# Optimization experiments

Hardware: AMD Instinct MI355X
Metric: run time of the kernel (lower is better)

The kernel has to match this reference:

```python
import jax, jax.numpy as jnp
import numpy as np

N_NODES = 100000


def gcn_conv(x, edge_index, W, b):
    """PyG GCNConv: add self-loops, symmetric deg^{-1/2} normalization,
    linear transform, scatter-add aggregation, then bias."""
    n = x.shape[0]
    loops = jnp.arange(n, dtype=edge_index.dtype)
    src = jnp.concatenate([edge_index[0], loops])  # [E+N]
    dst = jnp.concatenate([edge_index[1], loops])  # [E+N]
    # degree (with self-loops) of each target node
    deg = jax.ops.segment_sum(jnp.ones_like(dst, dtype=x.dtype), dst, num_segments=n)
    dinv = jnp.where(deg > 0, jax.lax.rsqrt(deg), 0.0)
    norm = dinv[src] * dinv[dst]  # [E+N]
    h = x @ W  # [N, out_dim] -- transform before aggregation
    msg = h[src] * norm[:, None]  # gather + normalize
    out = jax.ops.segment_sum(msg, dst, num_segments=n)  # scatter-add
    return out + b


def setup_inputs() -> dict:
    key = jax.random.key(0)
    ks = jax.random.split(key, 8)
    n, e, d_in, d_h = N_NODES, 1600000, 32, 64
    x = jax.random.normal(ks[0], (n, d_in), dtype=jnp.float32)
    edge_index = jax.random.randint(ks[1], (2, e), 0, n, dtype=jnp.int64)
    # Glorot-style init for GCN weights, uniform for linear layer
    W1 = jax.random.normal(ks[2], (d_in, d_h), dtype=jnp.float32) / np.sqrt(d_in)
    b1 = jnp.zeros((d_h,), dtype=jnp.float32)
    W2 = jax.random.normal(ks[3], (d_h, d_h), dtype=jnp.float32) / np.sqrt(d_h)
    b2 = jnp.zeros((d_h,), dtype=jnp.float32)
    Wo = jax.random.normal(ks[4], (d_h, 1), dtype=jnp.float32) / np.sqrt(d_h)
    bo = jnp.zeros((1,), dtype=jnp.float32)
    return {"x": x, "edge_index": edge_index, "W1": W1, "b1": b1,
            "W2": W2, "b2": b2, "Wo": Wo, "bo": bo}


def reference(x, edge_index, W1, b1, W2, b2, Wo, bo):
    h = jax.nn.relu(gcn_conv(x, edge_index, W1, b1))
    h = jax.nn.relu(gcn_conv(h, edge_index, W2, b2))
    logits = h @ Wo + bo  # [N, 1]
    return jax.nn.sigmoid(logits).squeeze(-1)  # [N]
```

## Files before the change

### kernel.cpp

```cpp
#include <hip/hip_runtime.h>

#define DH 64
#define DIN 32
#define BSH 8
#define BNODES 256
#define MAXB 1024
#define CAPSH 13
#define CAP (1 << CAPSH)

typedef unsigned short u16;
typedef unsigned int u32;
typedef float f32x2 __attribute__((ext_vector_type(2)));

__device__ __forceinline__ float bf2f(u16 u) {
    union { u32 i; float f; } x; x.i = ((u32)u) << 16; return x.f;
}
__device__ __forceinline__ u16 f2bf(float f) {
    union { float f; u32 i; } x; x.f = f;
    u32 r = x.i + 0x7fff + ((x.i >> 16) & 1);
    return (u16)(r >> 16);
}
__device__ __forceinline__ float bfl(u32 u) {
    union { u32 i; float f; } x; x.i = u << 16; return x.f;
}
__device__ __forceinline__ float bfh(u32 u) {
    union { u32 i; float f; } x; x.i = u & 0xffff0000u; return x.f;
}
__device__ __forceinline__ void pkacc(f32x2& a, u32 u) {
    f32x2 b;
    b[0] = bfl(u); b[1] = bfh(u);
    asm("v_pk_add_f32 %0, %1, %0" : "+v"(a) : "v"(b));
}

__global__ void __launch_bounds__(512) binA_k(
        const int* __restrict__ ei, int* __restrict__ gcnt,
        u32* __restrict__ pairs, int E, int n, int nbuck) {
    __shared__ int lhist[MAXB];
    __shared__ int lbase[MAXB];
    __shared__ int smode;
    int t = threadIdx.x;
    if (t < 64) {
        int v = (2 * t + 1 < 2 * E) ? ei[2 * t + 1] : 0;
        unsigned long long b = __ballot(v != 0);
        if (t == 0) smode = (b != 0ULL) ? 1 : 0;
    }
    for (int b = t; b < nbuck; b += 512) lhist[b] = 0;
    __syncthreads();
    int m = smode;
    unsigned un = (unsigned)n;
    int q0 = blockIdx.x * 512 + t;
    int qs = gridDim.x * 512;

    if (m && !(E & 3)) {
        const int4* d4 = (const int4*)(ei + E);
        for (int q = q0; q < (E >> 2); q += qs) {
            int4 d = d4[q];
            if ((unsigned)d.x < un) atomicAdd(&lhist[d.x >> BSH], 1);
            if ((unsigned)d.y < un) atomicAdd(&lhist[d.y >> BSH], 1);
            if ((unsigned)d.z < un) atomicAdd(&lhist[d.z >> BSH], 1);
            if ((unsigned)d.w < un) atomicAdd(&lhist[d.w >> BSH], 1);
        }
    } else if (!m && !(E & 1)) {
        const int4* d4 = (const int4*)(ei + 2 * E);
        for (int q = q0; q < (E >> 1); q += qs) {
            int4 d = d4[q];
            if ((unsigned)d.x < un) atomicAdd(&lhist[d.x >> BSH], 1);
            if ((unsigned)d.z < un) atomicAdd(&lhist[d.z >> BSH], 1);
        }
    } else {
        const int* dstp = m ? (ei + E) : (ei + 2 * E);
        int stride = m ? 1 : 2;
        for (int e = q0; e < E; e += qs) {
            int d = dstp[(size_t)e * stride];
            if ((unsigned)d < un) atomicAdd(&lhist[d >> BSH], 1);
        }
    }
    __syncthreads();
    for (int b = t; b < nbuck; b += 512) {
        int c = lhist[b];
        lbase[b] = c ? ((b << CAPSH) + atomicAdd(&gcnt[b], c)) : 0;
        lhist[b] = 0;
    }
    __syncthreads();
    #define EMIT(S, D)                                                     \
        if ((unsigned)(D) < un) {                                          \
            int sv = ((unsigned)(S) < un) ? (S) : 0;                       \
            int bb = (D) >> BSH;                                           \
            int off = atomicAdd(&lhist[bb], 1);                            \
            int pos = lbase[bb] + off;                                     \
            if (pos < ((bb + 1) << CAPSH))                                 \
                pairs[pos] = ((u32)sv << BSH) | (u32)((D) & (BNODES - 1)); \
        }
    if (m && !(E & 3)) {
        const int4* s4 = (const int4*)ei;
        const int4* d4 = (const int4*)(ei + E);
        for (int q = q0; q < (E >> 2); q += qs) {
            int4 s = s4[q]; int4 d = d4[q];
            EMIT(s.x, d.x) EMIT(s.y, d.y) EMIT(s.z, d.z) EMIT(s.w, d.w)
        }
    } else if (!m && !(E & 1)) {
        const int4* s4 = (const int4*)ei;
        const int4* d4 = (const int4*)(ei + 2 * E);
        for (int q = q0; q < (E >> 1); q += qs) {
            int4 s = s4[q]; int4 d = d4[q];
            EMIT(s.x, d.x) EMIT(s.z, d.z)
        }
    } else {
        const int* srcp = ei;
        const int* dstp = m ? (ei + E) : (ei + 2 * E);
        int stride = m ? 1 : 2;
        for (int e = q0; e < E; e += qs) {
            int d = dstp[(size_t)e * stride];
            int s = srcp[(size_t)e * stride];
            EMIT(s, d)
        }
    }
    #undef EMIT
}

__global__ void __launch_bounds__(512) csr_build_k(
        const u32* __restrict__ pairs, const int* __restrict__ gcnt,
        int* __restrict__ rstart, int* __restrict__ rend,
        int* __restrict__ col, float* __restrict__ dinv, int N) {
    __shared__ int cnt[BNODES];
    __shared__ int s[BNODES];
    int b = blockIdx.x, t = threadIdx.x;
    int base = b << CAPSH;
    int ec = gcnt[b]; if (ec > CAP) ec = CAP;
    int end = base + ec;
    if (t < BNODES) cnt[t] = 0;
    __syncthreads();
    for (int i = base + t; i < end; i += 512)
        atomicAdd(&cnt[pairs[i] & (BNODES - 1)], 1);
    __syncthreads();
    int v = (t < BNODES) ? cnt[t] : 0;
    if (t < BNODES) s[t] = v;
    __syncthreads();
    for (int off = 1; off < BNODES; off <<= 1) {
        int xsc = (t >= off && t < BNODES) ? s[t - off] : 0;
        __syncthreads();
        if (t < BNODES) s[t] += xsc;
        __syncthreads();
    }
    if (t < BNODES) {
        int excl = s[t] - v;
        int a = base + excl;
        int node = (b << BSH) + t;
        if (node < N) {
            rstart[node] = a;
            rend[node]   = a + v;
            dinv[node]   = rsqrtf((float)v + 1.0f);
        }
        cnt[t] = a;
    }
    __syncthreads();
    for (int i = base + t; i < end; i += 512) {
        u32 p = pairs[i];
        int pos = atomicAdd(&cnt[p & (BNODES - 1)], 1);
        col[pos] = (int)((p >> BSH) << 7);
    }
}

__global__ void __launch_bounds__(256) gemm1_k(
        const float* __restrict__ x, const float* __restrict__ W1,
        const float* __restrict__ dinv, u16* __restrict__ hp, int N) {
    __shared__ float Wl[DIN * DH];
    __shared__ float xl[16][DIN + 4];
    int t = threadIdx.x;
    {
        const float4* Wv = (const float4*)W1;
        float4* Wd = (float4*)Wl;
        #pragma unroll
        for (int r = 0; r < 2; r++) Wd[t + 256 * r] = Wv[t + 256 * r];
    }
    if (blockIdx.x == 0 && t < 32)
        ((float*)(hp + (size_t)N * DH))[t] = 0.f;
    if (t < 128) {
        int row = t >> 3, ck = (t & 7) * 4;
        int node = blockIdx.x * 16 + row;
        float4 vx = {0.f, 0.f, 0.f, 0.f};
        if (node < N)
            vx = *(const float4*)&x[(size_t)node * DIN + ck];
        *(float4*)&xl[row][ck] = vx;
    }
    __syncthreads();
    int lane = t & 63, w = t >> 6;
    int g = lane >> 4, c = lane & 15;
    int nl = w * 4 + g;
    int node = blockIdx.x * 16 + nl;
    const float* xr = xl[nl];
    float4 acc = {0.f, 0.f, 0.f, 0.f};
    #pragma unroll
    for (int k = 0; k < DIN; k++) {
        float xv = xr[k];
        float4 wv = *(const float4*)&Wl[k * DH + c * 4];
        acc.x += xv * wv.x; acc.y += xv * wv.y; acc.z += xv * wv.z; acc.w += xv * wv.w;
    }
    if (node < N) {
        float di = dinv[node];
        ushort4 o;
        o.x = f2bf(acc.x * di); o.y = f2bf(acc.y * di);
        o.z = f2bf(acc.z * di); o.w = f2bf(acc.w * di);
        *(ushort4*)&hp[(size_t)node * DH + c * 4] = o;
    }
}

__device__ __forceinline__ void edge_sum8p(const u16* __restrict__ hp,
                                           const int* __restrict__ colb,
                                           int start, int deg, int gl, int c,
                                           int sentb, f32x2* __restrict__ acc) {
    int dm = deg;
    dm = max(dm, __shfl_xor(dm, 8, 64));
    dm = max(dm, __shfl_xor(dm, 16, 64));
    dm = max(dm, __shfl_xor(dm, 32, 64));
    if (dm <= 0) return;
    const char* hpco = (const char*)hp + ((u32)c << 4);
    int cb = (c < deg) ? colb[start + c] : sentb;
    for (int base = 0; base < dm; base += 8) {
        int nb = base + 8;
        int cbn = sentb;
        if (nb < dm) cbn = (nb + c < deg) ? colb[start + nb + c] : sentb;
        int s0 = __shfl(cb, gl | 0, 64);
        int s1 = __shfl(cb, gl | 1, 64);
        int s2 = __shfl(cb, gl | 2, 64);
        int s3 = __shfl(cb, gl | 3, 64);
        int s4 = __shfl(cb, gl | 4, 64);
        int s5 = __shfl(cb, gl | 5, 64);
        int s6 = __shfl(cb, gl | 6, 64);
        int s7 = __shfl(cb, gl | 7, 64);
        uint4 v0 = *(const uint4*)(hpco + s0);
        uint4 v1 = *(const uint4*)(hpco + s1);
        uint4 v2 = *(const uint4*)(hpco + s2);
        uint4 v3 = *(const uint4*)(hpco + s3);
        uint4 v4 = *(const uint4*)(hpco + s4);
        uint4 v5 = *(const uint4*)(hpco + s5);
        uint4 v6 = *(const uint4*)(hpco + s6);
        uint4 v7 = *(const uint4*)(hpco + s7);
        pkacc(acc[0], v0.x); pkacc(acc[1], v0.y); pkacc(acc[2], v0.z); pkacc(acc[3], v0.w);
        pkacc(acc[0], v1.x); pkacc(acc[1], v1.y); pkacc(acc[2], v1.z); pkacc(acc[3], v1.w);
        pkacc(acc[0], v2.x); pkacc(acc[1], v2.y); pkacc(acc[2], v2.z); pkacc(acc[3], v2.w);
        pkacc(acc[0], v3.x); pkacc(acc[1], v3.y); pkacc(acc[2], v3.z); pkacc(acc[3], v3.w);
        pkacc(acc[0], v4.x); pkacc(acc[1], v4.y); pkacc(acc[2], v4.z); pkacc(acc[3], v4.w);
        pkacc(acc[0], v5.x); pkacc(acc[1], v5.y); pkacc(acc[2], v5.z); pkacc(acc[3], v5.w);
        pkacc(acc[0], v6.x); pkacc(acc[1], v6.y); pkacc(acc[2], v6.z); pkacc(acc[3], v6.w);
        pkacc(acc[0], v7.x); pkacc(acc[1], v7.y); pkacc(acc[2], v7.z); pkacc(acc[3], v7.w);
        cb = cbn;
    }
}

__global__ void __launch_bounds__(256) agg1_k(
        const u16* __restrict__ hp, const int* __restrict__ rstart,
        const int* __restrict__ rend, const int* __restrict__ col,
        const float* __restrict__ dinv, const float* __restrict__ b1,
        float* __restrict__ out1, int N) {
    int lane = threadIdx.x & 63;
    int g = lane >> 3, c = lane & 7, gl = g << 3;
    int node = blockIdx.x * 32 + (threadIdx.x >> 6) * 8 + g;
    int start = 0, deg = 0;
    if (node < N) { start = rstart[node]; deg = rend[node] - start; }
    f32x2 acc[4] = {{0.f,0.f},{0.f,0.f},{0.f,0.f},{0.f,0.f}};
    edge_sum8p(hp, col, start, deg, gl, c, N << 7, acc);
    if (node < N) {
        uint4 sv = *(const uint4*)&hp[(size_t)node * DH + c * 8];
        float di = dinv[node];
        float4 blo = *(const float4*)&b1[c * 8];
        float4 bhi = *(const float4*)&b1[c * 8 + 4];
        float4 lo, hi;
        lo.x = fmaxf((acc[0][0] + bfl(sv.x)) * di + blo.x, 0.f);
        lo.y = fmaxf((acc[0][1] + bfh(sv.x)) * di + blo.y, 0.f);
        lo.z = fmaxf((acc[1][0] + bfl(sv.y)) * di + blo.z, 0.f);
        lo.w = fmaxf((acc[1][1] + bfh(sv.y)) * di + blo.w, 0.f);
        hi.x = fmaxf((acc[2][0] + bfl(sv.z)) * di + bhi.x, 0.f);
        hi.y = fmaxf((acc[2][1] + bfh(sv.z)) * di + bhi.y, 0.f);
        hi.z = fmaxf((acc[3][0] + bfl(sv.w)) * di + bhi.z, 0.f);
        hi.w = fmaxf((acc[3][1] + bfh(sv.w)) * di + bhi.w, 0.f);
        *(float4*)&out1[(size_t)node * DH + c * 8]     = lo;
        *(float4*)&out1[(size_t)node * DH + c * 8 + 4] = hi;
    }
}

__global__ void __launch_bounds__(256) gemm2_k(
        const float* __restrict__ out1, const float* __restrict__ W2,
        const float* __restrict__ dinv, u16* __restrict__ hp2, int N) {
    __shared__ float Wl[DH * DH];
    __shared__ float xl[16][DH + 4];
    int t = threadIdx.x;
    {
        const float4* Wv = (const float4*)W2;
        float4* Wd = (float4*)Wl;
        #pragma unroll
        for (int r = 0; r < 4; r++) Wd[t + 256 * r] = Wv[t + 256 * r];
    }
    if (blockIdx.x == 0 && t < 32)
        ((float*)(hp2 + (size_t)N * DH))[t] = 0.f;
    {
        int row = t >> 4, ck = (t & 15) * 4;
        int node = blockIdx.x * 16 + row;
        float4 vx = {0.f, 0.f, 0.f, 0.f};
        if (node < N)
            vx = *(const float4*)&out1[(size_t)node * DH + ck];
        *(float4*)&xl[row][ck] = vx;
    }
    __syncthreads();
    int lane = t & 63, w = t >> 6;
    int g = lane >> 4, c = lane & 15;
    int nl = w * 4 + g;
    int node = blockIdx.x * 16 + nl;
    const float* xr = xl[nl];
    float4 acc = {0.f, 0.f, 0.f, 0.f};
    #pragma unroll
    for (int k = 0; k < DH; k++) {
        float xv = xr[k];
        float4 wv = *(const float4*)&Wl[k * DH + c * 4];
        acc.x += xv * wv.x; acc.y += xv * wv.y; acc.z += xv * wv.z; acc.w += xv * wv.w;
    }
    if (node < N) {
        float di = dinv[node];
        ushort4 o;
        o.x = f2bf(acc.x * di); o.y = f2bf(acc.y * di);
        o.z = f2bf(acc.z * di); o.w = f2bf(acc.w * di);
        *(ushort4*)&hp2[(size_t)node * DH + c * 4] = o;
    }
}

__global__ void __launch_bounds__(256) agg_head_k(
        const u16* __restrict__ hp, const int* __restrict__ rstart,
        const int* __restrict__ rend, const int* __restrict__ col,
        const float* __restrict__ dinv, const float* __restrict__ bias,
        const float* __restrict__ Wo, const float* __restrict__ bo,
        float* __restrict__ y, int N) {
    int lane = threadIdx.x & 63;
    int g = lane >> 3, c = lane & 7, gl = g << 3;
    int node = blockIdx.x * 32 + (threadIdx.x >> 6) * 8 + g;
    int start = 0, deg = 0;
    if (node < N) { start = rstart[node]; deg = rend[node] - start; }
    f32x2 acc[4] = {{0.f,0.f},{0.f,0.f},{0.f,0.f},{0.f,0.f}};
    edge_sum8p(hp, col, start, deg, gl, c, N << 7, acc);
    float t = 0.f;
    if (node < N) {
        uint4 sv = *(const uint4*)&hp[(size_t)node * DH + c * 8];
        float4 blo = *(const float4*)&bias[c * 8];
        float4 bhi = *(const float4*)&bias[c * 8 + 4];
        float4 wlo = *(const float4*)&Wo[c * 8];
        float4 whi = *(const float4*)&Wo[c * 8 + 4];
        float di = dinv[node];
        t = fmaxf((acc[0][0] + bfl(sv.x)) * di + blo.x, 0.f) * wlo.x
          + fmaxf((acc[0][1] + bfh(sv.x)) * di + blo.y, 0.f) * wlo.y
          + fmaxf((acc[1][0] + bfl(sv.y)) * di + blo.z, 0.f) * wlo.z
          + fmaxf((acc[1][1] + bfh(sv.y)) * di + blo.w, 0.f) * wlo.w
          + fmaxf((acc[2][0] + bfl(sv.z)) * di + bhi.x, 0.f) * whi.x
          + fmaxf((acc[2][1] + bfh(sv.z)) * di + bhi.y, 0.f) * whi.y
          + fmaxf((acc[3][0] + bfl(sv.w)) * di + bhi.z, 0.f) * whi.z
          + fmaxf((acc[3][1] + bfh(sv.w)) * di + bhi.w, 0.f) * whi.w;
    }
    t += __shfl_xor(t, 1, 64);
    t += __shfl_xor(t, 2, 64);
    t += __shfl_xor(t, 4, 64);
    if (c == 0 && node < N) {
        float z = t + bo[0];
        y[node] = 1.f / (1.f + __expf(-z));
    }
}

extern "C" void kernel_launch(void* const* d_in, const int* in_sizes, int n_in,
                              void* d_out, int out_size, void* d_ws, size_t ws_size,
                              hipStream_t stream) {
    const float* x  = (const float*)d_in[0];
    const int*   ei = (const int*)d_in[1];
    const float* W1 = (const float*)d_in[2];
    const float* b1 = (const float*)d_in[3];
    const float* W2 = (const float*)d_in[4];
    const float* b2 = (const float*)d_in[5];
    const float* Wo = (const float*)d_in[6];
    const float* bo = (const float*)d_in[7];
    float* y = (float*)d_out;

    int N = in_sizes[0] / DIN;
    int E = in_sizes[1] / 2;
    int nbuck = ((N - 1) >> BSH) + 1;

    char* ws = (char*)d_ws;
    size_t off = 0;
    auto alloc = [&](size_t bytes) { char* p = ws + off; off += (bytes + 255) & ~(size_t)255; return p; };
    int*   gcnt   = (int*)alloc(MAXB * 4);
    int*   rstart = (int*)alloc((size_t)N * 4);
    int*   rend   = (int*)alloc((size_t)N * 4);
    float* dinv   = (float*)alloc((size_t)N * 4);
    int*   col    = (int*)alloc(((size_t)nbuck << CAPSH) * 4);
    size_t pair_b = ((size_t)nbuck << CAPSH) * 4;
    size_t hp_b   = (size_t)N * DH * 2 + 256;
    char*  bufA   = (char*)alloc(pair_b > hp_b ? pair_b : hp_b);
    u16*   bufB   = (u16*)alloc(hp_b);
    float* out1   = (float*)alloc((size_t)N * DH * 4);
    u16*   hp    = (u16*)bufA;
    u32*   pairs = (u32*)bufA;

    hipMemsetAsync(gcnt, 0, (size_t)nbuck * 4, stream);
    binA_k<<<256, 512, 0, stream>>>(ei, gcnt, pairs, E, N, nbuck);
    csr_build_k<<<nbuck, 512, 0, stream>>>(pairs, gcnt, rstart, rend, col, dinv, N);
    gemm1_k<<<(N + 15) / 16, 256, 0, stream>>>(x, W1, dinv, hp, N);
    agg1_k<<<(N + 31) / 32, 256, 0, stream>>>(hp, rstart, rend, col, dinv, b1, out1, N);
    gemm2_k<<<(N + 15) / 16, 256, 0, stream>>>(out1, W2, dinv, bufB, N);
    agg_head_k<<<(N + 31) / 32, 256, 0, stream>>>(bufB, rstart, rend, col, dinv, b2, Wo, bo, y, N);
}
```

Measured before the change: 199.7 us.

## Register-cache CSR pairs, pack row bounds into int2, retune binning grid

The CSR build kernel now runs 1024 threads per bucket. Each thread loads up to eight pair entries into registers once and reuses them for both the counting pass and the scatter pass, so the second global read of pairs goes away. Row start and end are packed into a single int2 array, so each aggregation kernel does one 8-byte load per node. The binning kernel moves from 256 blocks of 512 threads to 1024 blocks of 256, which adds more global atomics on the bucket counters. The register path assumes at most 8192 entries per bucket, which holds because CAP is 8192.

```diff
diff --git a/kernel.cpp b/kernel.cpp
--- a/kernel.cpp
+++ b/kernel.cpp
@@ -32,7 +32,7 @@
     asm("v_pk_add_f32 %0, %1, %0" : "+v"(a) : "v"(b));
 }
 
-__global__ void __launch_bounds__(512) binA_k(
+__global__ void __launch_bounds__(256) binA_k(
         const int* __restrict__ ei, int* __restrict__ gcnt,
         u32* __restrict__ pairs, int E, int n, int nbuck) {
     __shared__ int lhist[MAXB];
@@ -44,12 +44,12 @@
         unsigned long long b = __ballot(v != 0);
         if (t == 0) smode = (b != 0ULL) ? 1 : 0;
     }
-    for (int b = t; b < nbuck; b += 512) lhist[b] = 0;
+    for (int b = t; b < nbuck; b += 256) lhist[b] = 0;
     __syncthreads();
     int m = smode;
     unsigned un = (unsigned)n;
-    int q0 = blockIdx.x * 512 + t;
-    int qs = gridDim.x * 512;
+    int q0 = blockIdx.x * 256 + t;
+    int qs = gridDim.x * 256;
 
     if (m && !(E & 3)) {
         const int4* d4 = (const int4*)(ei + E);
@@ -76,7 +76,7 @@
         }
     }
     __syncthreads();
-    for (int b = t; b < nbuck; b += 512) {
+    for (int b = t; b < nbuck; b += 256) {
         int c = lhist[b];
         lbase[b] = c ? ((b << CAPSH) + atomicAdd(&gcnt[b], c)) : 0;
         lhist[b] = 0;
@@ -118,9 +118,9 @@
     #undef EMIT
 }
 
-__global__ void __launch_bounds__(512) csr_build_k(
+__global__ void __launch_bounds__(1024) csr_build_k(
         const u32* __restrict__ pairs, const int* __restrict__ gcnt,
-        int* __restrict__ rstart, int* __restrict__ rend,
+        int2* __restrict__ rse,
         int* __restrict__ col, float* __restrict__ dinv, int N) {
     __shared__ int cnt[BNODES];
     __shared__ int s[BNODES];
@@ -130,8 +130,24 @@
     int end = base + ec;
     if (t < BNODES) cnt[t] = 0;
     __syncthreads();
-    for (int i = base + t; i < end; i += 512)
-        atomicAdd(&cnt[pairs[i] & (BNODES - 1)], 1);
+    u32 pr0, pr1, pr2, pr3, pr4, pr5, pr6, pr7;
+    #define IDX(K) (base + t + ((K) << 10))
+    pr0 = (IDX(0) < end) ? pairs[IDX(0)] : 0u;
+    pr1 = (IDX(1) < end) ? pairs[IDX(1)] : 0u;
+    pr2 = (IDX(2) < end) ? pairs[IDX(2)] : 0u;
+    pr3 = (IDX(3) < end) ? pairs[IDX(3)] : 0u;
+    pr4 = (IDX(4) < end) ? pairs[IDX(4)] : 0u;
+    pr5 = (IDX(5) < end) ? pairs[IDX(5)] : 0u;
+    pr6 = (IDX(6) < end) ? pairs[IDX(6)] : 0u;
+    pr7 = (IDX(7) < end) ? pairs[IDX(7)] : 0u;
+    if (IDX(0) < end) atomicAdd(&cnt[pr0 & (BNODES - 1)], 1);
+    if (IDX(1) < end) atomicAdd(&cnt[pr1 & (BNODES - 1)], 1);
+    if (IDX(2) < end) atomicAdd(&cnt[pr2 & (BNODES - 1)], 1);
+    if (IDX(3) < end) atomicAdd(&cnt[pr3 & (BNODES - 1)], 1);
+    if (IDX(4) < end) atomicAdd(&cnt[pr4 & (BNODES - 1)], 1);
+    if (IDX(5) < end) atomicAdd(&cnt[pr5 & (BNODES - 1)], 1);
+    if (IDX(6) < end) atomicAdd(&cnt[pr6 & (BNODES - 1)], 1);
+    if (IDX(7) < end) atomicAdd(&cnt[pr7 & (BNODES - 1)], 1);
     __syncthreads();
     int v = (t < BNODES) ? cnt[t] : 0;
     if (t < BNODES) s[t] = v;
@@ -147,18 +163,21 @@
         int a = base + excl;
         int node = (b << BSH) + t;
         if (node < N) {
-            rstart[node] = a;
-            rend[node]   = a + v;
-            dinv[node]   = rsqrtf((float)v + 1.0f);
+            rse[node]  = make_int2(a, a + v);
+            dinv[node] = rsqrtf((float)v + 1.0f);
         }
         cnt[t] = a;
     }
     __syncthreads();
-    for (int i = base + t; i < end; i += 512) {
-        u32 p = pairs[i];
-        int pos = atomicAdd(&cnt[p & (BNODES - 1)], 1);
-        col[pos] = (int)((p >> BSH) << 7);
-    }
+    #define SCAT(PR, K)                                                    \
+        if (IDX(K) < end) {                                                \
+            int pos = atomicAdd(&cnt[(PR) & (BNODES - 1)], 1);             \
+            col[pos] = (int)(((PR) >> BSH) << 7);                          \
+        }
+    SCAT(pr0, 0) SCAT(pr1, 1) SCAT(pr2, 2) SCAT(pr3, 3)
+    SCAT(pr4, 4) SCAT(pr5, 5) SCAT(pr6, 6) SCAT(pr7, 7)
+    #undef SCAT
+    #undef IDX
 }
 
 __global__ void __launch_bounds__(256) gemm1_k(
@@ -249,15 +268,15 @@
 }
 
 __global__ void __launch_bounds__(256) agg1_k(
-        const u16* __restrict__ hp, const int* __restrict__ rstart,
-        const int* __restrict__ rend, const int* __restrict__ col,
+        const u16* __restrict__ hp, const int2* __restrict__ rse,
+        const int* __restrict__ col,
         const float* __restrict__ dinv, const float* __restrict__ b1,
         float* __restrict__ out1, int N) {
     int lane = threadIdx.x & 63;
     int g = lane >> 3, c = lane & 7, gl = g << 3;
     int node = blockIdx.x * 32 + (threadIdx.x >> 6) * 8 + g;
     int start = 0, deg = 0;
-    if (node < N) { start = rstart[node]; deg = rend[node] - start; }
+    if (node < N) { int2 se = rse[node]; start = se.x; deg = se.y - se.x; }
     f32x2 acc[4] = {{0.f,0.f},{0.f,0.f},{0.f,0.f},{0.f,0.f}};
     edge_sum8p(hp, col, start, deg, gl, c, N << 7, acc);
     if (node < N) {
@@ -324,8 +343,8 @@
 }
 
 __global__ void __launch_bounds__(256) agg_head_k(
-        const u16* __restrict__ hp, const int* __restrict__ rstart,
-        const int* __restrict__ rend, const int* __restrict__ col,
+        const u16* __restrict__ hp, const int2* __restrict__ rse,
+        const int* __restrict__ col,
         const float* __restrict__ dinv, const float* __restrict__ bias,
         const float* __restrict__ Wo, const float* __restrict__ bo,
         float* __restrict__ y, int N) {
@@ -333,7 +352,7 @@
     int g = lane >> 3, c = lane & 7, gl = g << 3;
     int node = blockIdx.x * 32 + (threadIdx.x >> 6) * 8 + g;
     int start = 0, deg = 0;
-    if (node < N) { start = rstart[node]; deg = rend[node] - start; }
+    if (node < N) { int2 se = rse[node]; start = se.x; deg = se.y - se.x; }
     f32x2 acc[4] = {{0.f,0.f},{0.f,0.f},{0.f,0.f},{0.f,0.f}};
     edge_sum8p(hp, col, start, deg, gl, c, N << 7, acc);
     float t = 0.f;
@@ -383,8 +402,7 @@
     size_t off = 0;
     auto alloc = [&](size_t bytes) { char* p = ws + off; off += (bytes + 255) & ~(size_t)255; return p; };
     int*   gcnt   = (int*)alloc(MAXB * 4);
-    int*   rstart = (int*)alloc((size_t)N * 4);
-    int*   rend   = (int*)alloc((size_t)N * 4);
+    int2*  rse    = (int2*)alloc((size_t)N * 8);
     float* dinv   = (float*)alloc((size_t)N * 4);
     int*   col    = (int*)alloc(((size_t)nbuck << CAPSH) * 4);
     size_t pair_b = ((size_t)nbuck << CAPSH) * 4;
@@ -396,10 +414,10 @@
     u32*   pairs = (u32*)bufA;
 
     hipMemsetAsync(gcnt, 0, (size_t)nbuck * 4, stream);
-    binA_k<<<256, 512, 0, stream>>>(ei, gcnt, pairs, E, N, nbuck);
-    csr_build_k<<<nbuck, 512, 0, stream>>>(pairs, gcnt, rstart, rend, col, dinv, N);
+    binA_k<<<1024, 256, 0, stream>>>(ei, gcnt, pairs, E, N, nbuck);
+    csr_build_k<<<nbuck, 1024, 0, stream>>>(pairs, gcnt, rse, col, dinv, N);
     gemm1_k<<<(N + 15) / 16, 256, 0, stream>>>(x, W1, dinv, hp, N);
-    agg1_k<<<(N + 31) / 32, 256, 0, stream>>>(hp, rstart, rend, col, dinv, b1, out1, N);
+    agg1_k<<<(N + 31) / 32, 256, 0, stream>>>(hp, rse, col, dinv, b1, out1, N);
     gemm2_k<<<(N + 15) / 16, 256, 0, stream>>>(out1, W2, dinv, bufB, N);
-    agg_head_k<<<(N + 31) / 32, 256, 0, stream>>>(bufB, rstart, rend, col, dinv, b2, Wo, bo, y, N);
-}
+    agg_head_k<<<(N + 31) / 32, 256, 0, stream>>>(bufB, rse, col, dinv, b2, Wo, bo, y, N);
+}
```

New measurement: 220.0 us. 1.1x slower.
